# Kernel optimization log

Measured on AMD Instinct MI355X. Metric: run time of the kernel, lower is better.

Reference implementation:

```python
import jax, jax.numpy as jnp
import numpy as np

B, N, D, L, T = 64, 64, 128, 4, 10  # batch, atoms, hidden_dim, n_layers, n_atom_types
EPS = 1e-5


def setup_inputs() -> dict:
    key = jax.random.key(0)
    ks = jax.random.split(key, 10)
    def rn(k, shape, s=0.05):
        return jax.random.normal(k, shape, jnp.float32) * s
    return dict(
        positions=jax.random.normal(ks[0], (B, N, 3), jnp.float32),
        atomic_numbers=jax.random.randint(ks[1], (B, N), 0, T),
        embed=rn(ks[2], (T, D)),
        edge_w1=rn(ks[3], (L, 2 * D + 1, D)), edge_b1=jnp.zeros((L, D), jnp.float32),
        edge_w2=rn(ks[4], (L, D, D)), edge_b2=jnp.zeros((L, D), jnp.float32),
        node_w1=rn(ks[5], (L, 2 * D, D)), node_b1=jnp.zeros((L, D), jnp.float32),
        node_w2=rn(ks[6], (L, D, D)), node_b2=jnp.zeros((L, D), jnp.float32),
        ln_g=jnp.ones((L, D), jnp.float32), ln_b=jnp.zeros((L, D), jnp.float32),
        out_w=rn(ks[7], (D, 3)), out_b=jnp.zeros((3,), jnp.float32),
    )


def _layer(h, dist_sq, ew1, eb1, ew2, eb2, nw1, nb1, nw2, nb2, g, b):
    # edge_mlp first linear on cat([h_i, h_j, dist_sq]) == h@Wa (bcast over j)
    # + h@Wb (bcast over i) + dist_sq * w_d, avoiding materializing the concat.
    wa, wb, wd = ew1[:D], ew1[D:2 * D], ew1[2 * D]
    pre = (h @ wa)[:, :, None, :] + (h @ wb)[:, None, :, :] + dist_sq * wd + eb1  # [B,N,N,D]
    m_ij = jax.nn.silu(jax.nn.silu(pre) @ ew2 + eb2)
    m_i = m_ij.mean(axis=2)  # mean over j -> [B,N,D]
    # node_mlp on cat([h, m_i]) split the same way; dropout is eval-mode identity.
    h_out = jax.nn.silu(h @ nw1[:D] + m_i @ nw1[D:] + nb1) @ nw2 + nb2
    x = h + h_out
    mu = x.mean(-1, keepdims=True)
    var = ((x - mu) ** 2).mean(-1, keepdims=True)
    return (x - mu) / jnp.sqrt(var + EPS) * g + b


def reference(positions, atomic_numbers, embed, edge_w1, edge_b1, edge_w2, edge_b2,
              node_w1, node_b1, node_w2, node_b2, ln_g, ln_b, out_w, out_b):
    h = embed[atomic_numbers]  # [B,N,D]
    diff = positions[:, :, None, :] - positions[:, None, :, :]
    dist_sq = (diff ** 2).sum(-1, keepdims=True)  # [B,N,N,1]
    for i in range(L):
        h = _layer(h, dist_sq, edge_w1[i], edge_b1[i], edge_w2[i], edge_b2[i],
                   node_w1[i], node_b1[i], node_w2[i], node_b2[i], ln_g[i], ln_b[i])
    return h @ out_w + out_b  # [B,N,3]
```

## Files before the change

kernel.cpp:

```cpp
#include <hip/hip_runtime.h>
#include <hip/hip_fp16.h>


typedef _Float16 f16;
typedef _Float16 f16x8 __attribute__((ext_vector_type(8)));
typedef float f32x4 __attribute__((ext_vector_type(4)));

union H2x4 { f16x8 v; __half2 h[4]; };

__device__ __forceinline__ float bf2f(unsigned short u) {
    union { unsigned int i; float f; } v; v.i = ((unsigned int)u) << 16; return v.f;
}
__device__ __forceinline__ unsigned short f2bf(float f) {
    union { float f; unsigned int i; } v; v.f = f;
    unsigned int x = v.i;
    return (unsigned short)((x + 0x7fffu + ((x >> 16) & 1u)) >> 16);
}
__device__ __forceinline__ float silu_f(float x) {
    float e = __builtin_amdgcn_exp2f(-1.44269504088896f * x);
    return x * __builtin_amdgcn_rcpf(1.0f + e);
}
__device__ __forceinline__ __half2 silu_h2(__half2 x, __half2 kf, __half2 one2) {
    __half2 e = h2exp2(__hmul2(x, kf));
    return __hmul2(x, h2rcp(__hadd2(one2, e)));
}

struct Ptrs { const void* p[14]; };

__device__ __forceinline__ float ldf(const void* p, int i, int bf) {
    return bf ? bf2f(((const unsigned short*)p)[i]) : ((const float*)p)[i];
}

#define ELEM_TOTAL 393216
#define SMALL_TOTAL 17539

__global__ __launch_bounds__(256) void prep_kernel(
    Ptrs ptrs, f16* dst, float* sc)
{
    __shared__ int flgsh;
    int t = threadIdx.x;
    if (t < 64) {
        int ex = (((const unsigned short*)ptrs.p[0])[t * 2] >> 7) & 0xFF;
        unsigned long long m = __ballot(ex >= 110 && ex <= 135);
        if (t == 0) flgsh = (__popcll(m) >= 40) ? 1 : 0;
    }
    __syncthreads();
    int bf = flgsh;

    int gid = blockIdx.x * 256 + t;
    if (gid < ELEM_TOTAL) {
        int f = gid >> 3, j = gid & 7;
        int lay = f / 12288;
        int r   = f % 12288;
        const void* src; int base, rowoff = 0, r2;
        if (r < 6144) {
            int mat = r >> 11; r2 = r & 2047;
            if (mat == 0)      { src = ptrs.p[2]; base = lay * 32896; }
            else if (mat == 1) { src = ptrs.p[2]; base = lay * 32896; rowoff = 128; }
            else               { src = ptrs.p[4]; base = lay * 16384; }
        } else if (r < 10240) {
            r2 = r - 6144; src = ptrs.p[6]; base = lay * 32768;
        } else {
            r2 = r - 10240; src = ptrs.p[8]; base = lay * 16384;
        }
        int s = r2 >> 9, c = (r2 >> 6) & 7, l = r2 & 63;
        int row = rowoff + s * 32 + ((l >> 4) << 3) + j;
        int col = (c << 4) + (l & 15);
        dst[gid] = (f16)ldf(src, base + row * 128 + col, bf);
    } else {
        int sid = gid - ELEM_TOTAL;
        if (sid >= SMALL_TOTAL) return;
        const void* src; int i;
        if      (sid < 12288) { src = ptrs.p[0]; i = sid; }
        else if (sid < 13568) { src = ptrs.p[1]; i = sid - 12288; }
        else if (sid < 14080) { int k = sid - 13568;
                                src = ptrs.p[2]; i = (k >> 7) * 32896 + 32768 + (k & 127); }
        else if (sid < 14592) { src = ptrs.p[3];  i = sid - 14080; }
        else if (sid < 15104) { src = ptrs.p[5];  i = sid - 14592; }
        else if (sid < 15616) { src = ptrs.p[7];  i = sid - 15104; }
        else if (sid < 16128) { src = ptrs.p[9];  i = sid - 15616; }
        else if (sid < 16640) { src = ptrs.p[10]; i = sid - 16128; }
        else if (sid < 17152) { src = ptrs.p[11]; i = sid - 16640; }
        else if (sid < 17536) { src = ptrs.p[12]; i = sid - 17152; }
        else                  { src = ptrs.p[13]; i = sid - 17536; }
        sc[sid] = ldf(src, i, bf);
    }
}

__global__ __launch_bounds__(512) void embed_ab_kernel(
    const int* an, const float* sc, const f16* wa, const f16* wb,
    const float* eb1C, f16* h16, f16* a16, f16* b16)
{
    int t = threadIdx.x;
    int w = t >> 6, lane = t & 63;
    int row0 = blockIdx.x << 4;
    int m_ = lane & 15, q_ = lane >> 4;
    const float* emb = sc + 12288;
    int a = an[row0 + m_];
    a = a < 0 ? 0 : (a > 9 ? 9 : a);
    f16x8 afrag[4];
#pragma unroll
    for (int s = 0; s < 4; s++) {
        f32x4 u0 = *(const f32x4*)(emb + a * 128 + s * 32 + q_ * 8);
        f32x4 u1 = *(const f32x4*)(emb + a * 128 + s * 32 + q_ * 8 + 4);
        f16x8 hv;
#pragma unroll
        for (int e = 0; e < 4; e++) { hv[e] = (f16)u0[e]; hv[e + 4] = (f16)u1[e]; }
        afrag[s] = hv;
        if (w == 0)
            *(f16x8*)(h16 + (row0 + m_) * 128 + s * 32 + q_ * 8) = hv;
    }
    int c = w;
#pragma unroll
    for (int mat = 0; mat < 2; mat++) {
        const f16* W = mat ? wb : wa;
        f16* out     = mat ? b16 : a16;
        float init = mat ? 0.0f : eb1C[c * 16 + m_];
        f32x4 acc = { init, init, init, init };
#pragma unroll
        for (int s = 0; s < 4; s++) {
            f16x8 bfr = *(const f16x8*)(W + ((s * 8 + c) * 64 + lane) * 8);
            acc = __builtin_amdgcn_mfma_f32_16x16x32_f16(afrag[s], bfr, acc, 0, 0, 0);
        }
#pragma unroll
        for (int r = 0; r < 4; r++)
            out[(row0 + q_ * 4 + r) * 128 + c * 16 + m_] = (f16)acc[r];
    }
}

__global__ __launch_bounds__(512) void layer_kernel(
    const void* pos_raw, const float* sc, const f16* Wswz, int lay,
    f16* h16, f16* a16, const f16* bcur, f16* bnxt, void* out)
{
    __shared__ f16 ew2sl[16384];
    __shared__ f16 b_lds[64 * 136];
    __shared__ f16 ar_lds[8 * 136];
    __shared__ f16 m_lds[8 * 136];
    __shared__ __half dsqh[512];
    __shared__ f16 wd16[128];
    __shared__ float s1sh[8][16], s2sh[8][16];
    __shared__ float psh[8][16][3];
    __shared__ int flgsh;

    int t = threadIdx.x;
    int w = t >> 6, lane = t & 63;
    int m_ = lane & 15, q_ = lane >> 4;
    int m8 = m_ & 7;
    int c = w;
    int b  = blockIdx.x >> 3;
    int r0 = b * 64 + (blockIdx.x & 7) * 8;
    const int fin = (lay == 3);

    const f16* wl   = Wswz + lay * 98304;
    const f16* ew2s = wl + 32768;
    const f16* nw1s = wl + 49152;
    const f16* nw2s = wl + 81920;
    const float* posC = sc;
    const float* wdC  = sc + 13568 + lay * 128;
    const float* eb2C = sc + 14592 + lay * 128;
    const float* nb1C = sc + 15104 + lay * 128;
    const float* nb2C = sc + 15616 + lay * 128;
    const float* lngC = sc + 16128 + lay * 128;
    const float* lnbC = sc + 16640 + lay * 128;

    if (t < 64) {
        int ex = (((const unsigned short*)pos_raw)[t * 2] >> 7) & 0xFF;
        unsigned long long mk = __ballot(ex >= 110 && ex <= 135);
        if (t == 0) flgsh = (__popcll(mk) >= 40) ? 1 : 0;
    }

#pragma unroll
    for (int k = 0; k < 4; k++) {
        int idx = (k * 512 + t) * 8;
        *(f16x8*)(ew2sl + idx) = *(const f16x8*)(ew2s + idx);
    }
#pragma unroll
    for (int kk = 0; kk < 2; kk++) {
        int k = t + 512 * kk;
        int j = k >> 4, col0 = (k & 15) * 8;
        *(f16x8*)(b_lds + j * 136 + col0) =
            *(const f16x8*)(bcur + (b * 64 + j) * 128 + col0);
    }
    if (t < 128) {
        int row = t >> 4, col0 = (t & 15) * 8;
        *(f16x8*)(ar_lds + row * 136 + col0) =
            *(const f16x8*)(a16 + (r0 + row) * 128 + col0);
    }
    {
        int i = t >> 6, j = t & 63;
        int gi = r0 + i, gj = b * 64 + j;
        float dx = posC[gi * 3 + 0] - posC[gj * 3 + 0];
        float dy = posC[gi * 3 + 1] - posC[gj * 3 + 1];
        float dz = posC[gi * 3 + 2] - posC[gj * 3 + 2];
        dsqh[t] = __float2half_rn(dx * dx + dy * dy + dz * dz);
    }
    if (t < 128) wd16[t] = (f16)wdC[t];
    __syncthreads();

    {
        int i = w;
        f16x8 wdf[4];
#pragma unroll
        for (int s = 0; s < 4; s++)
            wdf[s] = *(const f16x8*)(wd16 + s * 32 + q_ * 8);
        float eb2v[8];
#pragma unroll
        for (int cc = 0; cc < 8; cc++) eb2v[cc] = eb2C[cc * 16 + m_];
        const __half2 kf   = __floats2half2_rn(-1.44269504f, -1.44269504f);
        const __half2 one2 = __floats2half2_rn(1.0f, 1.0f);
        f16x8 av[4];
#pragma unroll
        for (int s = 0; s < 4; s++)
            av[s] = *(const f16x8*)(ar_lds + i * 136 + s * 32 + q_ * 8);
        float msum[8] = { 0.f, 0.f, 0.f, 0.f, 0.f, 0.f, 0.f, 0.f };
#pragma unroll 1
        for (int mb = 0; mb < 4; mb++) {
            int j = mb * 16 + m_;
            __half dh = dsqh[i * 64 + j];
            __half2 ds2 = __halves2half2(dh, dh);
            f16x8 sf[4];
#pragma unroll
            for (int s = 0; s < 4; s++) {
                H2x4 av_, bv, wv, sv;
                av_.v = av[s];
                bv.v = *(const f16x8*)(b_lds + j * 136 + s * 32 + q_ * 8);
                wv.v = wdf[s];
#pragma unroll
                for (int e = 0; e < 4; e++) {
                    __half2 pre = __hfma2(ds2, wv.h[e],
                                          __hadd2(av_.h[e], bv.h[e]));
                    sv.h[e] = silu_h2(pre, kf, one2);
                }
                sf[s] = sv.v;
            }
#pragma unroll
            for (int cc = 0; cc < 8; cc++) {
                f32x4 acc = { eb2v[cc], eb2v[cc], eb2v[cc], eb2v[cc] };
#pragma unroll
                for (int s = 0; s < 4; s++) {
                    f16x8 wf = *(const f16x8*)(ew2sl + ((s * 8 + cc) * 64 + lane) * 8);
                    acc = __builtin_amdgcn_mfma_f32_16x16x32_f16(sf[s], wf, acc, 0, 0, 0);
                }
                msum[cc] += silu_f(acc[0]) + silu_f(acc[1])
                          + silu_f(acc[2]) + silu_f(acc[3]);
                __builtin_amdgcn_sched_barrier(0);
            }
        }
#pragma unroll
        for (int cc = 0; cc < 8; cc++) {
            float red = msum[cc];
            red += __shfl_xor(red, 16);
            red += __shfl_xor(red, 32);
            if (lane < 16)
                m_lds[i * 136 + cc * 16 + lane] = (f16)(red * 0.015625f);
        }
    }
    __syncthreads();

    f16x8 af2[8];
#pragma unroll
    for (int s = 0; s < 4; s++) {
        af2[s]     = *(const f16x8*)(h16 + (r0 + m8) * 128 + s * 32 + q_ * 8);
        af2[s + 4] = *(const f16x8*)(m_lds + m8 * 136 + s * 32 + q_ * 8);
    }
    f16* relay = ar_lds;
    {
        float e = nb1C[c * 16 + m_];
        f32x4 acc = { e, e, e, e };
#pragma unroll
        for (int s = 0; s < 8; s++) {
            f16x8 bv = *(const f16x8*)(nw1s + ((s * 8 + c) * 64 + lane) * 8);
            acc = __builtin_amdgcn_mfma_f32_16x16x32_f16(af2[s], bv, acc, 0, 0, 0);
        }
        if (q_ < 2)
#pragma unroll
            for (int r = 0; r < 4; r++)
                relay[(q_ * 4 + r) * 136 + c * 16 + m_] = (f16)silu_f(acc[r]);
    }
    __syncthreads();
    f16x8 uf[4];
#pragma unroll
    for (int s = 0; s < 4; s++)
        uf[s] = *(const f16x8*)(relay + m8 * 136 + s * 32 + q_ * 8);
    float x[4];
    {
        float e = nb2C[c * 16 + m_];
        f32x4 acc = { e, e, e, e };
#pragma unroll
        for (int s = 0; s < 4; s++) {
            f16x8 bv = *(const f16x8*)(nw2s + ((s * 8 + c) * 64 + lane) * 8);
            acc = __builtin_amdgcn_mfma_f32_16x16x32_f16(uf[s], bv, acc, 0, 0, 0);
        }
#pragma unroll
        for (int r = 0; r < 4; r++) {
            int row = q_ * 4 + r;
            x[r] = acc[r] + (float)h16[(r0 + (row & 7)) * 128 + c * 16 + m_];
        }
    }
    float s1p[4], s2p[4];
#pragma unroll
    for (int r = 0; r < 4; r++) { s1p[r] = x[r]; s2p[r] = x[r] * x[r]; }
#pragma unroll
    for (int msk = 1; msk < 16; msk <<= 1)
#pragma unroll
        for (int r = 0; r < 4; r++) {
            s1p[r] += __shfl_xor(s1p[r], msk);
            s2p[r] += __shfl_xor(s2p[r], msk);
        }
    if (m_ == 0)
#pragma unroll
        for (int r = 0; r < 4; r++) {
            s1sh[w][q_ * 4 + r] = s1p[r];
            s2sh[w][q_ * 4 + r] = s2p[r];
        }
    __syncthreads();
    float mu[4], rs[4];
#pragma unroll
    for (int r = 0; r < 4; r++) {
        int row = (q_ * 4 + r) & 7;
        float S1 = 0.f, S2 = 0.f;
#pragma unroll
        for (int w2 = 0; w2 < 8; w2++) { S1 += s1sh[w2][row]; S2 += s2sh[w2][row]; }
        mu[r] = S1 * (1.0f / 128.0f);
        float var = S2 * (1.0f / 128.0f) - mu[r] * mu[r];
        rs[r] = rsqrtf(var + 1e-5f);
    }

    if (!fin) {
        if (q_ < 2)
#pragma unroll
            for (int r = 0; r < 4; r++) {
                int col = c * 16 + m_;
                int row = r0 + q_ * 4 + r;
                float y = (x[r] - mu[r]) * rs[r] * lngC[col] + lnbC[col];
                h16[row * 128 + col] = (f16)y;
                relay[(q_ * 4 + r) * 136 + col] = (f16)y;
            }
        __syncthreads();
        f16x8 hf[4];
#pragma unroll
        for (int s = 0; s < 4; s++)
            hf[s] = *(const f16x8*)(relay + m8 * 136 + s * 32 + q_ * 8);
        const f16* wlN = Wswz + (lay + 1) * 98304;
        const float* eb1N = sc + 14080 + (lay + 1) * 128;
#pragma unroll
        for (int mat = 0; mat < 2; mat++) {
            const f16* W = mat ? (wlN + 16384) : wlN;
            float init = mat ? 0.0f : eb1N[c * 16 + m_];
            f32x4 acc = { init, init, init, init };
#pragma unroll
            for (int s = 0; s < 4; s++) {
                f16x8 bv = *(const f16x8*)(W + ((s * 8 + c) * 64 + lane) * 8);
                acc = __builtin_amdgcn_mfma_f32_16x16x32_f16(hf[s], bv, acc, 0, 0, 0);
            }
            if (q_ < 2)
#pragma unroll
                for (int r = 0; r < 4; r++) {
                    if (mat == 0)
                        a16[(r0 + q_ * 4 + r) * 128 + c * 16 + m_] = (f16)acc[r];
                    else
                        bnxt[(r0 + q_ * 4 + r) * 128 + c * 16 + m_] = (f16)acc[r];
                }
        }
    } else {
        const float* owC = sc + 17152;
        const float* obC = sc + 17536;
        float p[3][4];
#pragma unroll
        for (int r = 0; r < 4; r++) {
            int col = c * 16 + m_;
            float y = (x[r] - mu[r]) * rs[r] * lngC[col] + lnbC[col];
            p[0][r] = y * owC[col * 3 + 0];
            p[1][r] = y * owC[col * 3 + 1];
            p[2][r] = y * owC[col * 3 + 2];
        }
#pragma unroll
        for (int msk = 1; msk < 16; msk <<= 1)
#pragma unroll
            for (int k = 0; k < 3; k++)
#pragma unroll
                for (int r = 0; r < 4; r++)
                    p[k][r] += __shfl_xor(p[k][r], msk);
        if (m_ == 0)
#pragma unroll
            for (int r = 0; r < 4; r++)
#pragma unroll
                for (int k = 0; k < 3; k++)
                    psh[w][q_ * 4 + r][k] = p[k][r];
        __syncthreads();
        if (t < 8) {
            int row = r0 + t;
            int bf = flgsh;
#pragma unroll
            for (int k = 0; k < 3; k++) {
                float v = obC[k];
#pragma unroll
                for (int w2 = 0; w2 < 8; w2++) v += psh[w2][t][k];
                if (bf) ((unsigned short*)out)[row * 3 + k] = f2bf(v);
                else    ((float*)out)[row * 3 + k] = v;
            }
        }
    }
}

extern "C" void kernel_launch(void* const* d_in, const int* in_sizes, int n_in,
                              void* d_out, int out_size, void* d_ws, size_t ws_size,
                              hipStream_t stream)
{
    char* ws = (char*)d_ws;
    float* sc   = (float*)(ws + 1024);
    f16*   Wswz = (f16*)(ws + (128u << 10));
    f16*   h16  = (f16*)(ws + (1u << 20));
    f16*   a16  = (f16*)(ws + (2u << 20));
    f16*   b0   = (f16*)(ws + (3u << 20));
    f16*   b1   = (f16*)(ws + (4u << 20));

    Ptrs ptrs;
    const int src_idx[14] = {0, 2, 3, 4, 5, 6, 7, 8, 9, 10, 11, 12, 13, 14};
    for (int k = 0; k < 14; k++) ptrs.p[k] = d_in[src_idx[k]];

    prep_kernel<<<1605, 256, 0, stream>>>(ptrs, Wswz, sc);
    embed_ab_kernel<<<256, 512, 0, stream>>>((const int*)d_in[1], sc, Wswz,
                                             Wswz + 16384, sc + 14080,
                                             h16, a16, b0);
    for (int lay = 0; lay < 4; lay++) {
        const f16* bcur = (lay & 1) ? b1 : b0;
        f16*       bnxt = (lay & 1) ? b0 : b1;
        layer_kernel<<<512, 512, 0, stream>>>(d_in[0], sc, Wswz, lay,
                                              h16, a16, bcur, bnxt, d_out);
    }
}
```

Before: 203.3 us.

## Double layer kernel block to 1024 threads, splitting edge output columns across wave pairs

The layer kernel now launches 16 waves per block instead of 8. Each pair of waves shares one node row i, and each wave computes half of the edge MLP output columns. The node MLP and layer-norm phases run only on the first 8 waves. Register arrays that were cached before (the a row, wd, and node inputs) are now re-read from LDS to cut register pressure under launch_bounds(1024, 8). The goal is more latency hiding and more MFMA parallelism in the dominant edge phase. The cost is that every wave pair recomputes the same pre-activation silu on the VALU, and LDS traffic goes up.

```diff
diff --git a/kernel.cpp b/kernel.cpp
--- a/kernel.cpp
+++ b/kernel.cpp
@@ -128,7 +128,7 @@
     }
 }
 
-__global__ __launch_bounds__(512) void layer_kernel(
+__global__ __launch_bounds__(1024, 8) void layer_kernel(
     const void* pos_raw, const float* sc, const f16* Wswz, int lay,
     f16* h16, f16* a16, const f16* bcur, f16* bnxt, void* out)
 {
@@ -146,7 +146,6 @@
     int w = t >> 6, lane = t & 63;
     int m_ = lane & 15, q_ = lane >> 4;
     int m8 = m_ & 7;
-    int c = w;
     int b  = blockIdx.x >> 3;
     int r0 = b * 64 + (blockIdx.x & 7) * 8;
     const int fin = (lay == 3);
@@ -170,14 +169,12 @@
     }
 
 #pragma unroll
-    for (int k = 0; k < 4; k++) {
-        int idx = (k * 512 + t) * 8;
+    for (int k = 0; k < 2; k++) {
+        int idx = (k * 1024 + t) * 8;
         *(f16x8*)(ew2sl + idx) = *(const f16x8*)(ew2s + idx);
     }
-#pragma unroll
-    for (int kk = 0; kk < 2; kk++) {
-        int k = t + 512 * kk;
-        int j = k >> 4, col0 = (k & 15) * 8;
+    {
+        int j = t >> 4, col0 = (t & 15) * 8;
         *(f16x8*)(b_lds + j * 136 + col0) =
             *(const f16x8*)(bcur + (b * 64 + j) * 128 + col0);
     }
@@ -186,7 +183,7 @@
         *(f16x8*)(ar_lds + row * 136 + col0) =
             *(const f16x8*)(a16 + (r0 + row) * 128 + col0);
     }
-    {
+    if (t < 512) {
         int i = t >> 6, j = t & 63;
         int gi = r0 + i, gj = b * 64 + j;
         float dx = posC[gi * 3 + 0] - posC[gj * 3 + 0];
@@ -194,25 +191,18 @@
         float dz = posC[gi * 3 + 2] - posC[gj * 3 + 2];
         dsqh[t] = __float2half_rn(dx * dx + dy * dy + dz * dz);
     }
-    if (t < 128) wd16[t] = (f16)wdC[t];
+    if (t >= 512 && t < 640) wd16[t - 512] = (f16)wdC[t - 512];
     __syncthreads();
 
     {
-        int i = w;
-        f16x8 wdf[4];
-#pragma unroll
-        for (int s = 0; s < 4; s++)
-            wdf[s] = *(const f16x8*)(wd16 + s * 32 + q_ * 8);
-        float eb2v[8];
-#pragma unroll
-        for (int cc = 0; cc < 8; cc++) eb2v[cc] = eb2C[cc * 16 + m_];
+        int i   = w >> 1;
+        int ccb = (w & 1) * 4;
+        float eb2v[4];
+#pragma unroll
+        for (int cc = 0; cc < 4; cc++) eb2v[cc] = eb2C[(ccb + cc) * 16 + m_];
         const __half2 kf   = __floats2half2_rn(-1.44269504f, -1.44269504f);
         const __half2 one2 = __floats2half2_rn(1.0f, 1.0f);
-        f16x8 av[4];
-#pragma unroll
-        for (int s = 0; s < 4; s++)
-            av[s] = *(const f16x8*)(ar_lds + i * 136 + s * 32 + q_ * 8);
-        float msum[8] = { 0.f, 0.f, 0.f, 0.f, 0.f, 0.f, 0.f, 0.f };
+        float msum[4] = { 0.f, 0.f, 0.f, 0.f };
 #pragma unroll 1
         for (int mb = 0; mb < 4; mb++) {
             int j = mb * 16 + m_;
@@ -222,9 +212,9 @@
 #pragma unroll
             for (int s = 0; s < 4; s++) {
                 H2x4 av_, bv, wv, sv;
-                av_.v = av[s];
-                bv.v = *(const f16x8*)(b_lds + j * 136 + s * 32 + q_ * 8);
-                wv.v = wdf[s];
+                av_.v = *(const f16x8*)(ar_lds + i * 136 + s * 32 + q_ * 8);
+                bv.v  = *(const f16x8*)(b_lds + j * 136 + s * 32 + q_ * 8);
+                wv.v  = *(const f16x8*)(wd16 + s * 32 + q_ * 8);
 #pragma unroll
                 for (int e = 0; e < 4; e++) {
                     __half2 pre = __hfma2(ds2, wv.h[e],
@@ -234,11 +224,12 @@
                 sf[s] = sv.v;
             }
 #pragma unroll
-            for (int cc = 0; cc < 8; cc++) {
+            for (int cc = 0; cc < 4; cc++) {
                 f32x4 acc = { eb2v[cc], eb2v[cc], eb2v[cc], eb2v[cc] };
 #pragma unroll
                 for (int s = 0; s < 4; s++) {
-                    f16x8 wf = *(const f16x8*)(ew2sl + ((s * 8 + cc) * 64 + lane) * 8);
+                    f16x8 wf = *(const f16x8*)(ew2sl +
+                        ((s * 8 + ccb + cc) * 64 + lane) * 8);
                     acc = __builtin_amdgcn_mfma_f32_16x16x32_f16(sf[s], wf, acc, 0, 0, 0);
                 }
                 msum[cc] += silu_f(acc[0]) + silu_f(acc[1])
@@ -247,30 +238,32 @@
             }
         }
 #pragma unroll
-        for (int cc = 0; cc < 8; cc++) {
+        for (int cc = 0; cc < 4; cc++) {
             float red = msum[cc];
             red += __shfl_xor(red, 16);
             red += __shfl_xor(red, 32);
             if (lane < 16)
-                m_lds[i * 136 + cc * 16 + lane] = (f16)(red * 0.015625f);
+                m_lds[i * 136 + (ccb + cc) * 16 + lane] = (f16)(red * 0.015625f);
         }
     }
     __syncthreads();
 
-    f16x8 af2[8];
-#pragma unroll
-    for (int s = 0; s < 4; s++) {
-        af2[s]     = *(const f16x8*)(h16 + (r0 + m8) * 128 + s * 32 + q_ * 8);
-        af2[s + 4] = *(const f16x8*)(m_lds + m8 * 136 + s * 32 + q_ * 8);
-    }
     f16* relay = ar_lds;
-    {
+    int c = w;
+    if (w < 8) {
         float e = nb1C[c * 16 + m_];
         f32x4 acc = { e, e, e, e };
 #pragma unroll
-        for (int s = 0; s < 8; s++) {
+        for (int s = 0; s < 4; s++) {
+            f16x8 af = *(const f16x8*)(h16 + (r0 + m8) * 128 + s * 32 + q_ * 8);
             f16x8 bv = *(const f16x8*)(nw1s + ((s * 8 + c) * 64 + lane) * 8);
-            acc = __builtin_amdgcn_mfma_f32_16x16x32_f16(af2[s], bv, acc, 0, 0, 0);
+            acc = __builtin_amdgcn_mfma_f32_16x16x32_f16(af, bv, acc, 0, 0, 0);
+        }
+#pragma unroll
+        for (int s = 0; s < 4; s++) {
+            f16x8 af = *(const f16x8*)(m_lds + m8 * 136 + s * 32 + q_ * 8);
+            f16x8 bv = *(const f16x8*)(nw1s + (((s + 4) * 8 + c) * 64 + lane) * 8);
+            acc = __builtin_amdgcn_mfma_f32_16x16x32_f16(af, bv, acc, 0, 0, 0);
         }
         if (q_ < 2)
 #pragma unroll
@@ -278,56 +271,54 @@
                 relay[(q_ * 4 + r) * 136 + c * 16 + m_] = (f16)silu_f(acc[r]);
     }
     __syncthreads();
-    f16x8 uf[4];
-#pragma unroll
-    for (int s = 0; s < 4; s++)
-        uf[s] = *(const f16x8*)(relay + m8 * 136 + s * 32 + q_ * 8);
-    float x[4];
-    {
+    float x[4], mu[4], rs[4];
+    if (w < 8) {
         float e = nb2C[c * 16 + m_];
         f32x4 acc = { e, e, e, e };
 #pragma unroll
         for (int s = 0; s < 4; s++) {
+            f16x8 uf = *(const f16x8*)(relay + m8 * 136 + s * 32 + q_ * 8);
             f16x8 bv = *(const f16x8*)(nw2s + ((s * 8 + c) * 64 + lane) * 8);
-            acc = __builtin_amdgcn_mfma_f32_16x16x32_f16(uf[s], bv, acc, 0, 0, 0);
+            acc = __builtin_amdgcn_mfma_f32_16x16x32_f16(uf, bv, acc, 0, 0, 0);
         }
 #pragma unroll
         for (int r = 0; r < 4; r++) {
             int row = q_ * 4 + r;
             x[r] = acc[r] + (float)h16[(r0 + (row & 7)) * 128 + c * 16 + m_];
         }
-    }
-    float s1p[4], s2p[4];
-#pragma unroll
-    for (int r = 0; r < 4; r++) { s1p[r] = x[r]; s2p[r] = x[r] * x[r]; }
-#pragma unroll
-    for (int msk = 1; msk < 16; msk <<= 1)
+        float s1p[4], s2p[4];
+#pragma unroll
+        for (int r = 0; r < 4; r++) { s1p[r] = x[r]; s2p[r] = x[r] * x[r]; }
+#pragma unroll
+        for (int msk = 1; msk < 16; msk <<= 1)
+#pragma unroll
+            for (int r = 0; r < 4; r++) {
+                s1p[r] += __shfl_xor(s1p[r], msk);
+                s2p[r] += __shfl_xor(s2p[r], msk);
+            }
+        if (m_ == 0)
+#pragma unroll
+            for (int r = 0; r < 4; r++) {
+                s1sh[w][q_ * 4 + r] = s1p[r];
+                s2sh[w][q_ * 4 + r] = s2p[r];
+            }
+    }
+    __syncthreads();
+    if (w < 8) {
 #pragma unroll
         for (int r = 0; r < 4; r++) {
-            s1p[r] += __shfl_xor(s1p[r], msk);
-            s2p[r] += __shfl_xor(s2p[r], msk);
-        }
-    if (m_ == 0)
-#pragma unroll
-        for (int r = 0; r < 4; r++) {
-            s1sh[w][q_ * 4 + r] = s1p[r];
-            s2sh[w][q_ * 4 + r] = s2p[r];
-        }
-    __syncthreads();
-    float mu[4], rs[4];
-#pragma unroll
-    for (int r = 0; r < 4; r++) {
-        int row = (q_ * 4 + r) & 7;
-        float S1 = 0.f, S2 = 0.f;
-#pragma unroll
-        for (int w2 = 0; w2 < 8; w2++) { S1 += s1sh[w2][row]; S2 += s2sh[w2][row]; }
-        mu[r] = S1 * (1.0f / 128.0f);
-        float var = S2 * (1.0f / 128.0f) - mu[r] * mu[r];
-        rs[r] = rsqrtf(var + 1e-5f);
+            int row = (q_ * 4 + r) & 7;
+            float S1 = 0.f, S2 = 0.f;
+#pragma unroll
+            for (int w2 = 0; w2 < 8; w2++) { S1 += s1sh[w2][row]; S2 += s2sh[w2][row]; }
+            mu[r] = S1 * (1.0f / 128.0f);
+            float var = S2 * (1.0f / 128.0f) - mu[r] * mu[r];
+            rs[r] = rsqrtf(var + 1e-5f);
+        }
     }
 
     if (!fin) {
-        if (q_ < 2)
+        if (w < 8 && q_ < 2)
 #pragma unroll
             for (int r = 0; r < 4; r++) {
                 int col = c * 16 + m_;
@@ -337,58 +328,59 @@
                 relay[(q_ * 4 + r) * 136 + col] = (f16)y;
             }
         __syncthreads();
-        f16x8 hf[4];
-#pragma unroll
-        for (int s = 0; s < 4; s++)
-            hf[s] = *(const f16x8*)(relay + m8 * 136 + s * 32 + q_ * 8);
-        const f16* wlN = Wswz + (lay + 1) * 98304;
-        const float* eb1N = sc + 14080 + (lay + 1) * 128;
-#pragma unroll
-        for (int mat = 0; mat < 2; mat++) {
-            const f16* W = mat ? (wlN + 16384) : wlN;
-            float init = mat ? 0.0f : eb1N[c * 16 + m_];
-            f32x4 acc = { init, init, init, init };
-#pragma unroll
-            for (int s = 0; s < 4; s++) {
-                f16x8 bv = *(const f16x8*)(W + ((s * 8 + c) * 64 + lane) * 8);
-                acc = __builtin_amdgcn_mfma_f32_16x16x32_f16(hf[s], bv, acc, 0, 0, 0);
-            }
-            if (q_ < 2)
-#pragma unroll
-                for (int r = 0; r < 4; r++) {
-                    if (mat == 0)
-                        a16[(r0 + q_ * 4 + r) * 128 + c * 16 + m_] = (f16)acc[r];
-                    else
-                        bnxt[(r0 + q_ * 4 + r) * 128 + c * 16 + m_] = (f16)acc[r];
+        if (w < 8) {
+            const f16* wlN = Wswz + (lay + 1) * 98304;
+            const float* eb1N = sc + 14080 + (lay + 1) * 128;
+#pragma unroll
+            for (int mat = 0; mat < 2; mat++) {
+                const f16* W = mat ? (wlN + 16384) : wlN;
+                float init = mat ? 0.0f : eb1N[c * 16 + m_];
+                f32x4 acc = { init, init, init, init };
+#pragma unroll
+                for (int s = 0; s < 4; s++) {
+                    f16x8 hf = *(const f16x8*)(relay + m8 * 136 + s * 32 + q_ * 8);
+                    f16x8 bv = *(const f16x8*)(W + ((s * 8 + c) * 64 + lane) * 8);
+                    acc = __builtin_amdgcn_mfma_f32_16x16x32_f16(hf, bv, acc, 0, 0, 0);
                 }
+                if (q_ < 2)
+#pragma unroll
+                    for (int r = 0; r < 4; r++) {
+                        if (mat == 0)
+                            a16[(r0 + q_ * 4 + r) * 128 + c * 16 + m_] = (f16)acc[r];
+                        else
+                            bnxt[(r0 + q_ * 4 + r) * 128 + c * 16 + m_] = (f16)acc[r];
+                    }
+            }
         }
     } else {
-        const float* owC = sc + 17152;
-        const float* obC = sc + 17536;
-        float p[3][4];
-#pragma unroll
-        for (int r = 0; r < 4; r++) {
-            int col = c * 16 + m_;
-            float y = (x[r] - mu[r]) * rs[r] * lngC[col] + lnbC[col];
-            p[0][r] = y * owC[col * 3 + 0];
-            p[1][r] = y * owC[col * 3 + 1];
-            p[2][r] = y * owC[col * 3 + 2];
-        }
-#pragma unroll
-        for (int msk = 1; msk < 16; msk <<= 1)
-#pragma unroll
-            for (int k = 0; k < 3; k++)
+        if (w < 8) {
+            const float* owC = sc + 17152;
+            float p[3][4];
+#pragma unroll
+            for (int r = 0; r < 4; r++) {
+                int col = c * 16 + m_;
+                float y = (x[r] - mu[r]) * rs[r] * lngC[col] + lnbC[col];
+                p[0][r] = y * owC[col * 3 + 0];
+                p[1][r] = y * owC[col * 3 + 1];
+                p[2][r] = y * owC[col * 3 + 2];
+            }
+#pragma unroll
+            for (int msk = 1; msk < 16; msk <<= 1)
+#pragma unroll
+                for (int k = 0; k < 3; k++)
+#pragma unroll
+                    for (int r = 0; r < 4; r++)
+                        p[k][r] += __shfl_xor(p[k][r], msk);
+            if (m_ == 0)
 #pragma unroll
                 for (int r = 0; r < 4; r++)
-                    p[k][r] += __shfl_xor(p[k][r], msk);
-        if (m_ == 0)
-#pragma unroll
-            for (int r = 0; r < 4; r++)
-#pragma unroll
-                for (int k = 0; k < 3; k++)
-                    psh[w][q_ * 4 + r][k] = p[k][r];
+#pragma unroll
+                    for (int k = 0; k < 3; k++)
+                        psh[w][q_ * 4 + r][k] = p[k][r];
+        }
         __syncthreads();
         if (t < 8) {
+            const float* obC = sc + 17536;
             int row = r0 + t;
             int bf = flgsh;
 #pragma unroll
@@ -426,7 +418,7 @@
     for (int lay = 0; lay < 4; lay++) {
         const f16* bcur = (lay & 1) ? b1 : b0;
         f16*       bnxt = (lay & 1) ? b0 : b1;
-        layer_kernel<<<512, 512, 0, stream>>>(d_in[0], sc, Wswz, lay,
-                                              h16, a16, bcur, bnxt, d_out);
-    }
-}
+        layer_kernel<<<512, 1024, 0, stream>>>(d_in[0], sc, Wswz, lay,
+                                               h16, a16, bcur, bnxt, d_out);
+    }
+}
```

Result: slower. 235.6 us (+15.9%).
